# Kernel tuning notes

Hardware: AMD Instinct MI355X
Metric: run time of the kernel (lower is better)

## Reference

```python
import jax, jax.numpy as jnp
import numpy as np

B, N, L, D, H, NLAYERS, V = 8, 1024, 16, 256, 4, 2, 32000
DH = D // H  # per-head dim


def setup_inputs() -> dict:
    key = jax.random.key(0)
    ks = jax.random.split(key, 7)
    cfg_adj = jax.random.randint(ks[0], (B, N, N), 0, 2, dtype=jnp.int32)
    cfg_nodes = jax.random.randint(ks[1], (B, N, L), 0, V, dtype=jnp.int32)
    cfg_len = jax.random.randint(ks[2], (B,), 1, N + 1, dtype=jnp.int32)
    emb = jax.random.normal(ks[3], (V, D), jnp.float32) * 0.02
    # xavier-ish scale for per-head projections and attention vectors
    W = jax.random.normal(ks[4], (NLAYERS, H, D, DH), jnp.float32) * np.float32(np.sqrt(2.0 / (D + DH)))
    a_src = jax.random.normal(ks[5], (NLAYERS, H, DH), jnp.float32) * 0.1
    a_dst = jax.random.normal(ks[6], (NLAYERS, H, DH), jnp.float32) * 0.1
    ln_scale = jnp.ones((NLAYERS, D), jnp.float32)
    ln_bias = jnp.zeros((NLAYERS, D), jnp.float32)
    return {"cfg_adj": cfg_adj, "cfg_nodes": cfg_nodes, "cfg_len": cfg_len,
            "emb": emb, "W": W, "a_src": a_src, "a_dst": a_dst,
            "ln_scale": ln_scale, "ln_bias": ln_bias}


def _layer_norm(x, scale, bias, eps=1e-5):
    mu = jnp.mean(x, axis=-1, keepdims=True)
    var = jnp.var(x, axis=-1, keepdims=True)
    return (x - mu) * jax.lax.rsqrt(var + eps) * scale + bias


def reference(cfg_adj, cfg_nodes, cfg_len, emb, W, a_src, a_dst, ln_scale, ln_bias):
    # node features: mean over token embeddings (dropout is identity in eval)
    node_feat = emb[cfg_nodes].mean(axis=2)                       # (B,N,D)
    # add self-loops once (repeated add+clamp in the original is idempotent)
    adj = jnp.minimum(cfg_adj + jnp.eye(N, dtype=cfg_adj.dtype)[None], 1)
    neg_mask = (adj == 0)[:, None]                                # (B,1,N,N)
    h = node_feat
    for l in range(NLAYERS):
        Wh = jnp.einsum('bnd,hdk->bhnk', h, W[l])                 # (B,H,N,DH)
        src = jnp.einsum('bhnk,hk->bhn', Wh, a_src[l])            # (B,H,N)
        dst = jnp.einsum('bhnk,hk->bhn', Wh, a_dst[l])            # (B,H,N)
        e = jax.nn.leaky_relu(src[:, :, :, None] + dst[:, :, None, :], 0.2)
        e = jnp.where(neg_mask, jnp.float32(-1e9), e)             # masked fill
        alpha = jax.nn.softmax(e, axis=-1)                        # (B,H,N,N)
        h_prime = jnp.einsum('bhnm,bhmk->bhnk', alpha, Wh)        # (B,H,N,DH)
        h_cat = jnp.transpose(h_prime, (0, 2, 1, 3)).reshape(B, N, D)
        h = _layer_norm(h + h_cat, ln_scale[l], ln_bias[l])
    return h, cfg_len
```

## Files before the change

kernel.cpp:

```cpp
#include <hip/hip_runtime.h>
#include <math.h>

#define B 8
#define N 1024
#define L 16
#define D 256
#define H 4
#define DH 64
#define NLAYERS 2
#define V 32000

typedef __attribute__((ext_vector_type(8))) short short8;
typedef __attribute__((ext_vector_type(4))) float f32x4;

union U8 { uint4 u; short8 s; };

__device__ inline unsigned short f2bf(float x) {
    unsigned u = __float_as_uint(x);
    u = (u + 0x7fff + ((u >> 16) & 1)) >> 16;
    return (unsigned short)u;
}
__device__ inline float bf2f(unsigned short x) {
    return __uint_as_float(((unsigned)x) << 16);
}


#define PACK_BLK 2048
#define WT_BLK   (NLAYERS * H * 4)
#define EMB_BLK  500
#define PRE1_GRID (PACK_BLK + WT_BLK + EMB_BLK + 1)

__global__ __launch_bounds__(256) void k_pre1(const int* __restrict__ adj,
                                              const float* __restrict__ W,
                                              const int* __restrict__ len,
                                              const float* __restrict__ emb,
                                              unsigned long long* __restrict__ pack,
                                              unsigned short* __restrict__ WT_sw,
                                              unsigned short* __restrict__ emb_bf,
                                              float* __restrict__ out_len) {
    int bid = blockIdx.x;
    int t = threadIdx.x;
    if (bid < PACK_BLK) {
        int row = bid * 4 + (t >> 6);
        int lane = t & 63;
        int n = row & (N - 1);
        const int* arow = adj + (long)row * N;
        unsigned long long* prow = pack + (size_t)row * 16;
        int g16 = lane & 15;
#pragma unroll
        for (int it = 0; it < 4; ++it) {
            int m0 = it * 256 + lane * 4;
            int4 a = *(const int4*)(arow + m0);
            unsigned nib = (unsigned)((a.x != 0) || (m0 == n))
                         | ((unsigned)((a.y != 0) || (m0 + 1 == n)) << 1)
                         | ((unsigned)((a.z != 0) || (m0 + 2 == n)) << 2)
                         | ((unsigned)((a.w != 0) || (m0 + 3 == n)) << 3);
            unsigned long long v = (unsigned long long)nib << (g16 * 4);
            v |= __shfl_xor(v, 1, 64);
            v |= __shfl_xor(v, 2, 64);
            v |= __shfl_xor(v, 4, 64);
            v |= __shfl_xor(v, 8, 64);
            if (g16 == 0) prow[it * 4 + (lane >> 4)] = v;
        }
    } else if (bid < PACK_BLK + WT_BLK) {
        int idx = bid - PACK_BLK;
        int lh = idx >> 2, q = idx & 3;
        const float* Wl = W + (size_t)lh * D * DH;
        int dh = t & 63;
        int d0 = q * 64 + (t >> 6) * 16;
#pragma unroll
        for (int i = 0; i < 16; ++i) {
            int d = d0 + i;
            WT_sw[(((size_t)lh * 8 + (d >> 5)) * 64 + dh) * 32 + (d & 31)] = f2bf(Wl[(size_t)d * DH + dh]);
        }
    } else if (bid < PACK_BLK + WT_BLK + EMB_BLK) {
        size_t base = (size_t)(bid - PACK_BLK - WT_BLK) * 16384 + (size_t)t * 4;
#pragma unroll
        for (int i = 0; i < 16; ++i) {
            float4 v = *(const float4*)&emb[base + (size_t)i * 1024];
            ushort4 o;
            o.x = f2bf(v.x); o.y = f2bf(v.y); o.z = f2bf(v.z); o.w = f2bf(v.w);
            *(ushort4*)&emb_bf[base + (size_t)i * 1024] = o;
        }
    } else {
        if (t < B) out_len[t] = (float)len[t];
    }
}

__global__ __launch_bounds__(256) void k_nodefeat(const int* __restrict__ nodes,
                                                  const unsigned short* __restrict__ emb_bf,
                                                  float* __restrict__ h,
                                                  unsigned short* __restrict__ h_sw) {
    int row = blockIdx.x * 8 + (threadIdx.x >> 5);
    int lane32 = threadIdx.x & 31;
    int d8 = lane32 * 8;
    const int* np = nodes + row * L;
    float s[8] = {};
#pragma unroll
    for (int l = 0; l < L; ++l) {
        short8 v = *(const short8*)&emb_bf[(size_t)np[l] * D + d8];
#pragma unroll
        for (int k = 0; k < 8; ++k) s[k] += bf2f((unsigned short)v[k]);
    }
#pragma unroll
    for (int k = 0; k < 8; ++k) s[k] *= (1.0f / L);
    *(float4*)&h[(size_t)row * D + d8] = make_float4(s[0], s[1], s[2], s[3]);
    *(float4*)&h[(size_t)row * D + d8 + 4] = make_float4(s[4], s[5], s[6], s[7]);
    int b = row >> 10, n = row & 1023;
    unsigned short o[8];
#pragma unroll
    for (int k = 0; k < 8; ++k) o[k] = f2bf(s[k]);
    *(short8*)&h_sw[(((size_t)b * 64 + (n >> 4)) * 8 + (d8 >> 5)) * 512 + (n & 15) * 32 + (d8 & 31)] =
        *(short8*)o;
}

__global__ __launch_bounds__(256) void k_wh(const unsigned short* __restrict__ h_sw,
                                            const unsigned short* __restrict__ WT_l,
                                            const float* __restrict__ asrc_l,
                                            const float* __restrict__ adst_l,
                                            unsigned short* __restrict__ WhT,
                                            float* __restrict__ srcv,
                                            float* __restrict__ dstv) {
    __shared__ float red[4][16][68];
    int bt = blockIdx.x;
    int hh = blockIdx.y;
    int b = bt >> 6;
    int nt = bt & 63;
    int n0 = nt * 16;
    int tid = threadIdx.x;
    int w = tid >> 6, lane = tid & 63;
    int rowLane = lane & 15, quad = lane >> 4;
    int bh = b * H + hh;
    const unsigned short* abase = h_sw + (((size_t)b * 64 + nt) * 8) * 512 + rowLane * 32 + quad * 8;
    const unsigned short* bbase = WT_l + ((size_t)hh * 8) * 2048 + rowLane * 32 + quad * 8;
    f32x4 acc[4] = {};
#pragma unroll
    for (int kk = 0; kk < 2; ++kk) {
        int kc = w * 2 + kk;
        short8 af = *(const short8*)(abase + kc * 512);
#pragma unroll
        for (int c = 0; c < 4; ++c) {
            short8 bf = *(const short8*)(bbase + kc * 2048 + c * 512);
            acc[c] = __builtin_amdgcn_mfma_f32_16x16x32_bf16(af, bf, acc[c], 0, 0, 0);
        }
    }
#pragma unroll
    for (int c = 0; c < 4; ++c)
#pragma unroll
        for (int r = 0; r < 4; ++r)
            red[w][quad * 4 + r][c * 16 + rowLane] = acc[c][r];
    __syncthreads();
    int dh = tid >> 2, j4 = tid & 3;
    float v[4];
#pragma unroll
    for (int i = 0; i < 4; ++i)
        v[i] = red[0][j4 * 4 + i][dh] + red[1][j4 * 4 + i][dh] + red[2][j4 * 4 + i][dh] + red[3][j4 * 4 + i][dh];
    ushort4 o;
    o.x = f2bf(v[0]); o.y = f2bf(v[1]); o.z = f2bf(v[2]); o.w = f2bf(v[3]);
    *(ushort4*)&WhT[(((size_t)bh * 32 + (n0 >> 5)) * 64 + dh) * 32 + (n0 & 31) + j4 * 4] = o;
    float as = asrc_l[hh * DH + dh];
    float ad = adst_l[hh * DH + dh];
    float* ps = &red[0][0][0];
    float* pd = ps + 16 * 68;
    __syncthreads();
#pragma unroll
    for (int i = 0; i < 4; ++i) {
        ps[(j4 * 4 + i) * 68 + dh] = v[i] * as;
        pd[(j4 * 4 + i) * 68 + dh] = v[i] * ad;
    }
    __syncthreads();
    int nl = tid >> 4, g = tid & 15;
    float4 s4 = *(float4*)&ps[nl * 68 + g * 4];
    float4 t4 = *(float4*)&pd[nl * 68 + g * 4];
    float s1 = s4.x + s4.y + s4.z + s4.w;
    float d1 = t4.x + t4.y + t4.z + t4.w;
#pragma unroll
    for (int off = 8; off; off >>= 1) {
        s1 += __shfl_xor(s1, off, 16);
        d1 += __shfl_xor(d1, off, 16);
    }
    if (g == 0) {
        srcv[bh * N + n0 + nl] = s1;
        dstv[bh * N + n0 + nl] = d1;
    }
}

__global__ __launch_bounds__(256) void k_attn(const unsigned long long* __restrict__ pack,
                                              const float* __restrict__ srcv,
                                              const float* __restrict__ dstv,
                                              const unsigned short* __restrict__ WhT,
                                              float* __restrict__ hp) {
    __shared__ float red[4][16][68];
    __shared__ float ssum[4][16];
    float* dsts = &red[0][0][0];

    int tid = threadIdx.x;
    int bt = blockIdx.x;
    int bh = bt >> 6;
    int n0 = (bt & 63) * 16;
    int b = bh >> 2;
    int w = tid >> 6, lane = tid & 63;
    int rowLane = lane & 15, quad = lane >> 4;
    int n = n0 + rowLane;

    {
        float4 v = *(const float4*)(dstv + bh * N + w * 256 + lane * 4);
        *(float4*)(dsts + w * 256 + lane * 4) = v;
    }
    const uint4* pbp = (const uint4*)((const unsigned char*)(pack + ((size_t)(b * N + n)) * 16) + w * 32);
    uint4 pbv0 = pbp[0];
    uint4 pbv1 = pbp[1];
    float src = srcv[bh * N + n];
    float mx = src > 0.f ? src : 0.2f * src;

    unsigned words[8] = {pbv0.x, pbv0.y, pbv0.z, pbv0.w, pbv1.x, pbv1.y, pbv1.z, pbv1.w};
    const unsigned short* wbase = WhT + ((size_t)bh * 32) * 2048 + rowLane * 32 + quad * 8;
    f32x4 acc[4] = {};
    float sum0 = 0.f, sum1 = 0.f;
#pragma unroll
    for (int t2 = 0; t2 < 8; ++t2) {
        unsigned bits = (words[t2] >> (quad * 8)) & 0xffu;
        float4 d0 = *(const float4*)(dsts + w * 256 + t2 * 32 + quad * 8);
        float4 d1 = *(const float4*)(dsts + w * 256 + t2 * 32 + quad * 8 + 4);
        float dd[8] = {d0.x, d0.y, d0.z, d0.w, d1.x, d1.y, d1.z, d1.w};
        unsigned pk[4];
#pragma unroll
        for (int j2 = 0; j2 < 4; ++j2) {
            float ea = src + dd[2 * j2];
            float eb = src + dd[2 * j2 + 1];
            ea = ea > 0.f ? ea : 0.2f * ea;
            eb = eb > 0.f ? eb : 0.2f * eb;
            float pa = ((bits >> (2 * j2)) & 1) ? __expf(ea - mx) : 0.f;
            float pb = ((bits >> (2 * j2 + 1)) & 1) ? __expf(eb - mx) : 0.f;
            sum0 += pa; sum1 += pb;
            pk[j2] = (__float_as_uint(pb) & 0xffff0000u) | (__float_as_uint(pa) >> 16);
        }
        U8 u; u.u = make_uint4(pk[0], pk[1], pk[2], pk[3]);
        short8 af = u.s;
        const unsigned short* tb = wbase + (size_t)(w * 8 + t2) * 2048;
        acc[0] = __builtin_amdgcn_mfma_f32_16x16x32_bf16(af, *(const short8*)(tb + 0 * 512), acc[0], 0, 0, 0);
        acc[1] = __builtin_amdgcn_mfma_f32_16x16x32_bf16(af, *(const short8*)(tb + 1 * 512), acc[1], 0, 0, 0);
        acc[2] = __builtin_amdgcn_mfma_f32_16x16x32_bf16(af, *(const short8*)(tb + 2 * 512), acc[2], 0, 0, 0);
        acc[3] = __builtin_amdgcn_mfma_f32_16x16x32_bf16(af, *(const short8*)(tb + 3 * 512), acc[3], 0, 0, 0);
    }
    float sum = sum0 + sum1;
    sum += __shfl_xor(sum, 16, 64);
    sum += __shfl_xor(sum, 32, 64);
    if (quad == 0) ssum[w][rowLane] = sum;
    __syncthreads();
#pragma unroll
    for (int c = 0; c < 4; ++c)
#pragma unroll
        for (int r = 0; r < 4; ++r)
            red[w][quad * 4 + r][c * 16 + rowLane] = acc[c][r];
    __syncthreads();
    int row = tid >> 4, col4 = (tid & 15) * 4;
    float4 s = make_float4(0.f, 0.f, 0.f, 0.f);
#pragma unroll
    for (int ww = 0; ww < 4; ++ww) {
        float4 v = *(const float4*)&red[ww][row][col4];
        s.x += v.x; s.y += v.y; s.z += v.z; s.w += v.w;
    }
    float invr = 1.0f / (ssum[0][row] + ssum[1][row] + ssum[2][row] + ssum[3][row]);
    s.x *= invr; s.y *= invr; s.z *= invr; s.w *= invr;
    *(float4*)&hp[((size_t)bh * N + n0 + row) * DH + col4] = s;
}

__global__ __launch_bounds__(256) void k_ln(const float* __restrict__ h,
                                            const float* __restrict__ hp,
                                            const float* __restrict__ scale,
                                            const float* __restrict__ bias,
                                            float* __restrict__ out,
                                            unsigned short* __restrict__ h_sw,
                                            int layer, int has_next) {
    __shared__ float red[8];
    int bn = blockIdx.x;
    int b = bn >> 10, n = bn & 1023;
    int c = threadIdx.x;
    int hh = c >> 6, k = c & 63;
    float x = h[(size_t)bn * D + c] + hp[((size_t)(b * H + hh) * N + n) * DH + k];
    float s = x, s2 = x * x;
#pragma unroll
    for (int off = 32; off; off >>= 1) {
        s += __shfl_xor(s, off, 64);
        s2 += __shfl_xor(s2, off, 64);
    }
    int w = c >> 6, lane = c & 63;
    if (lane == 0) { red[w] = s; red[4 + w] = s2; }
    __syncthreads();
    s = red[0] + red[1] + red[2] + red[3];
    s2 = red[4] + red[5] + red[6] + red[7];
    float mu = s * (1.0f / D);
    float var = s2 * (1.0f / D) - mu * mu;
    float r = rsqrtf(var + 1e-5f);
    float y = (x - mu) * r * scale[layer * D + c] + bias[layer * D + c];
    out[(size_t)bn * D + c] = y;
    if (has_next)
        h_sw[(((size_t)b * 64 + (n >> 4)) * 8 + (c >> 5)) * 512 + (n & 15) * 32 + (c & 31)] = f2bf(y);
}

extern "C" void kernel_launch(void* const* d_in, const int* in_sizes, int n_in,
                              void* d_out, int out_size, void* d_ws, size_t ws_size,
                              hipStream_t stream) {
    const int* cfg_adj = (const int*)d_in[0];
    const int* cfg_nodes = (const int*)d_in[1];
    const int* cfg_len = (const int*)d_in[2];
    const float* emb = (const float*)d_in[3];
    const float* W = (const float*)d_in[4];
    const float* a_src = (const float*)d_in[5];
    const float* a_dst = (const float*)d_in[6];
    const float* ln_scale = (const float*)d_in[7];
    const float* ln_bias = (const float*)d_in[8];
    float* out = (float*)d_out;
    float* ws = (float*)d_ws;

    float* h = ws;
    float* hp = h + (size_t)B * N * D;
    float* srcv = hp + (size_t)B * H * N * DH;
    float* dstv = srcv + (size_t)B * H * N;
    unsigned short* h_sw = (unsigned short*)(dstv + (size_t)B * H * N);
    unsigned short* WhT = h_sw + (size_t)B * N * D;
    unsigned short* WT_sw = WhT + (size_t)B * H * DH * N;
    unsigned short* emb_bf = WT_sw + (size_t)NLAYERS * H * DH * D;
    unsigned long long* pack = (unsigned long long*)(emb_bf + (size_t)V * D);

    k_pre1<<<PRE1_GRID, 256, 0, stream>>>(cfg_adj, W, cfg_len, emb, pack, WT_sw,
                                          emb_bf, out + (size_t)B * N * D);
    k_nodefeat<<<B * N / 8, 256, 0, stream>>>(cfg_nodes, emb_bf, h, h_sw);
    for (int l = 0; l < NLAYERS; ++l) {
        k_wh<<<dim3(B * 64, H), 256, 0, stream>>>(
            h_sw, WT_sw + (size_t)l * H * 8 * 2048,
            a_src + (size_t)l * H * DH, a_dst + (size_t)l * H * DH,
            WhT, srcv, dstv);
        k_attn<<<B * H * 64, 256, 0, stream>>>(pack, srcv, dstv, WhT, hp);
        k_ln<<<B * N, 256, 0, stream>>>(h, hp, ln_scale, ln_bias,
                                        (l == NLAYERS - 1) ? out : h, h_sw,
                                        l, l < NLAYERS - 1 ? 1 : 0);
    }
}
```

Before: 203.1 us.

## Fuse node-feature gather with Wh projection and attention with layernorm

```diff
diff --git a/kernel.cpp b/kernel.cpp
--- a/kernel.cpp
+++ b/kernel.cpp
@@ -87,141 +87,177 @@
     }
 }
 
-__global__ __launch_bounds__(256) void k_nodefeat(const int* __restrict__ nodes,
-                                                  const unsigned short* __restrict__ emb_bf,
-                                                  float* __restrict__ h,
-                                                  unsigned short* __restrict__ h_sw) {
-    int row = blockIdx.x * 8 + (threadIdx.x >> 5);
-    int lane32 = threadIdx.x & 31;
-    int d8 = lane32 * 8;
-    const int* np = nodes + row * L;
-    float s[8] = {};
-#pragma unroll
-    for (int l = 0; l < L; ++l) {
-        short8 v = *(const short8*)&emb_bf[(size_t)np[l] * D + d8];
-#pragma unroll
-        for (int k = 0; k < 8; ++k) s[k] += bf2f((unsigned short)v[k]);
-    }
-#pragma unroll
-    for (int k = 0; k < 8; ++k) s[k] *= (1.0f / L);
-    *(float4*)&h[(size_t)row * D + d8] = make_float4(s[0], s[1], s[2], s[3]);
-    *(float4*)&h[(size_t)row * D + d8 + 4] = make_float4(s[4], s[5], s[6], s[7]);
-    int b = row >> 10, n = row & 1023;
-    unsigned short o[8];
-#pragma unroll
-    for (int k = 0; k < 8; ++k) o[k] = f2bf(s[k]);
-    *(short8*)&h_sw[(((size_t)b * 64 + (n >> 4)) * 8 + (d8 >> 5)) * 512 + (n & 15) * 32 + (d8 & 31)] =
-        *(short8*)o;
-}
-
-__global__ __launch_bounds__(256) void k_wh(const unsigned short* __restrict__ h_sw,
-                                            const unsigned short* __restrict__ WT_l,
-                                            const float* __restrict__ asrc_l,
-                                            const float* __restrict__ adst_l,
-                                            unsigned short* __restrict__ WhT,
-                                            float* __restrict__ srcv,
-                                            float* __restrict__ dstv) {
-    __shared__ float red[4][16][68];
-    int bt = blockIdx.x;
-    int hh = blockIdx.y;
-    int b = bt >> 6;
-    int nt = bt & 63;
-    int n0 = nt * 16;
-    int tid = threadIdx.x;
-    int w = tid >> 6, lane = tid & 63;
+__device__ inline void wh_epilogue(float (*wtmp)[16][68], const f32x4* acc,
+                                   const float* asrc_l, const float* adst_l,
+                                   unsigned short* WhT, float* srcv, float* dstv,
+                                   int b, int n0, int tid) {
+    int hh = tid >> 6, lane = tid & 63;
     int rowLane = lane & 15, quad = lane >> 4;
     int bh = b * H + hh;
+    float as[4], ad[4];
+#pragma unroll
+    for (int c = 0; c < 4; ++c) {
+        as[c] = asrc_l[hh * DH + c * 16 + rowLane];
+        ad[c] = adst_l[hh * DH + c * 16 + rowLane];
+    }
+#pragma unroll
+    for (int rr = 0; rr < 4; ++rr) {
+        float sp = acc[0][rr] * as[0] + acc[1][rr] * as[1] + acc[2][rr] * as[2] + acc[3][rr] * as[3];
+        float dp = acc[0][rr] * ad[0] + acc[1][rr] * ad[1] + acc[2][rr] * ad[2] + acc[3][rr] * ad[3];
+#pragma unroll
+        for (int off = 8; off; off >>= 1) {
+            sp += __shfl_xor(sp, off, 16);
+            dp += __shfl_xor(dp, off, 16);
+        }
+        if (rowLane == 0) {
+            srcv[(size_t)bh * N + n0 + quad * 4 + rr] = sp;
+            dstv[(size_t)bh * N + n0 + quad * 4 + rr] = dp;
+        }
+    }
+#pragma unroll
+    for (int c = 0; c < 4; ++c)
+#pragma unroll
+        for (int rr = 0; rr < 4; ++rr)
+            wtmp[hh][quad * 4 + rr][c * 16 + rowLane] = acc[c][rr];
+    __syncthreads();
+    int hh2 = tid >> 6, dh = tid & 63;
+    int bh2 = b * H + hh2;
+#pragma unroll
+    for (int j4 = 0; j4 < 4; ++j4) {
+        ushort4 o;
+        o.x = f2bf(wtmp[hh2][j4 * 4 + 0][dh]);
+        o.y = f2bf(wtmp[hh2][j4 * 4 + 1][dh]);
+        o.z = f2bf(wtmp[hh2][j4 * 4 + 2][dh]);
+        o.w = f2bf(wtmp[hh2][j4 * 4 + 3][dh]);
+        *(ushort4*)&WhT[(((size_t)bh2 * 32 + (n0 >> 5)) * 64 + dh) * 32 + (n0 & 31) + j4 * 4] = o;
+    }
+}
+
+__global__ __launch_bounds__(256) void k_feat_wh(const int* __restrict__ nodes,
+                                                 const unsigned short* __restrict__ emb_bf,
+                                                 const unsigned short* __restrict__ WT_l,
+                                                 const float* __restrict__ asrc_l,
+                                                 const float* __restrict__ adst_l,
+                                                 float* __restrict__ h,
+                                                 unsigned short* __restrict__ WhT,
+                                                 float* __restrict__ srcv,
+                                                 float* __restrict__ dstv) {
+    __shared__ int ndl[256];
+    __shared__ unsigned short a_lds[8][16][40];
+    __shared__ float wtmp[4][16][68];
+    int bt = blockIdx.x;
+    int b = bt >> 6, nt = bt & 63, n0 = nt * 16;
+    int tid = threadIdx.x;
+    ndl[tid] = nodes[((size_t)(b * N + n0)) * L + tid];
+    __syncthreads();
+    int r = tid >> 4, g = tid & 15;
+    float s[16] = {};
+#pragma unroll
+    for (int l = 0; l < L; ++l) {
+        int tok = ndl[r * 16 + l];
+        short8 v0 = *(const short8*)&emb_bf[(size_t)tok * D + g * 16];
+        short8 v1 = *(const short8*)&emb_bf[(size_t)tok * D + g * 16 + 8];
+#pragma unroll
+        for (int k = 0; k < 8; ++k) {
+            s[k] += bf2f((unsigned short)v0[k]);
+            s[8 + k] += bf2f((unsigned short)v1[k]);
+        }
+    }
+#pragma unroll
+    for (int k = 0; k < 16; ++k) s[k] *= (1.0f / L);
+    float* hrow = h + ((size_t)(b * N + n0 + r)) * D + g * 16;
+    *(float4*)(hrow + 0) = make_float4(s[0], s[1], s[2], s[3]);
+    *(float4*)(hrow + 4) = make_float4(s[4], s[5], s[6], s[7]);
+    *(float4*)(hrow + 8) = make_float4(s[8], s[9], s[10], s[11]);
+    *(float4*)(hrow + 12) = make_float4(s[12], s[13], s[14], s[15]);
+    unsigned short ob[16];
+#pragma unroll
+    for (int k = 0; k < 16; ++k) ob[k] = f2bf(s[k]);
+    *(short8*)&a_lds[g >> 1][r][(g & 1) * 16] = *(short8*)&ob[0];
+    *(short8*)&a_lds[g >> 1][r][(g & 1) * 16 + 8] = *(short8*)&ob[8];
+    __syncthreads();
+    int hh = tid >> 6, lane = tid & 63;
+    int rowLane = lane & 15, quad = lane >> 4;
+    const unsigned short* bbase = WT_l + ((size_t)hh * 8) * 2048 + rowLane * 32 + quad * 8;
+    f32x4 acc[4] = {};
+#pragma unroll
+    for (int kc = 0; kc < 8; ++kc) {
+        short8 af = *(const short8*)&a_lds[kc][rowLane][quad * 8];
+#pragma unroll
+        for (int c = 0; c < 4; ++c)
+            acc[c] = __builtin_amdgcn_mfma_f32_16x16x32_bf16(af, *(const short8*)(bbase + kc * 2048 + c * 512), acc[c], 0, 0, 0);
+    }
+    wh_epilogue(wtmp, acc, asrc_l, adst_l, WhT, srcv, dstv, b, n0, tid);
+}
+
+__global__ __launch_bounds__(256) void k_wh1(const unsigned short* __restrict__ h_sw,
+                                             const unsigned short* __restrict__ WT_l,
+                                             const float* __restrict__ asrc_l,
+                                             const float* __restrict__ adst_l,
+                                             unsigned short* __restrict__ WhT,
+                                             float* __restrict__ srcv,
+                                             float* __restrict__ dstv) {
+    __shared__ float wtmp[4][16][68];
+    int bt = blockIdx.x;
+    int b = bt >> 6, nt = bt & 63, n0 = nt * 16;
+    int tid = threadIdx.x;
+    int hh = tid >> 6, lane = tid & 63;
+    int rowLane = lane & 15, quad = lane >> 4;
     const unsigned short* abase = h_sw + (((size_t)b * 64 + nt) * 8) * 512 + rowLane * 32 + quad * 8;
     const unsigned short* bbase = WT_l + ((size_t)hh * 8) * 2048 + rowLane * 32 + quad * 8;
     f32x4 acc[4] = {};
 #pragma unroll
-    for (int kk = 0; kk < 2; ++kk) {
-        int kc = w * 2 + kk;
+    for (int kc = 0; kc < 8; ++kc) {
         short8 af = *(const short8*)(abase + kc * 512);
 #pragma unroll
-        for (int c = 0; c < 4; ++c) {
-            short8 bf = *(const short8*)(bbase + kc * 2048 + c * 512);
-            acc[c] = __builtin_amdgcn_mfma_f32_16x16x32_bf16(af, bf, acc[c], 0, 0, 0);
-        }
-    }
-#pragma unroll
-    for (int c = 0; c < 4; ++c)
-#pragma unroll
-        for (int r = 0; r < 4; ++r)
-            red[w][quad * 4 + r][c * 16 + rowLane] = acc[c][r];
-    __syncthreads();
-    int dh = tid >> 2, j4 = tid & 3;
-    float v[4];
-#pragma unroll
-    for (int i = 0; i < 4; ++i)
-        v[i] = red[0][j4 * 4 + i][dh] + red[1][j4 * 4 + i][dh] + red[2][j4 * 4 + i][dh] + red[3][j4 * 4 + i][dh];
-    ushort4 o;
-    o.x = f2bf(v[0]); o.y = f2bf(v[1]); o.z = f2bf(v[2]); o.w = f2bf(v[3]);
-    *(ushort4*)&WhT[(((size_t)bh * 32 + (n0 >> 5)) * 64 + dh) * 32 + (n0 & 31) + j4 * 4] = o;
-    float as = asrc_l[hh * DH + dh];
-    float ad = adst_l[hh * DH + dh];
-    float* ps = &red[0][0][0];
-    float* pd = ps + 16 * 68;
-    __syncthreads();
+        for (int c = 0; c < 4; ++c)
+            acc[c] = __builtin_amdgcn_mfma_f32_16x16x32_bf16(af, *(const short8*)(bbase + kc * 2048 + c * 512), acc[c], 0, 0, 0);
+    }
+    wh_epilogue(wtmp, acc, asrc_l, adst_l, WhT, srcv, dstv, b, n0, tid);
+}
+
+__global__ __launch_bounds__(256) void k_attn_ln(const unsigned long long* __restrict__ pack,
+                                                 const float* __restrict__ srcv,
+                                                 const float* __restrict__ dstv,
+                                                 const unsigned short* __restrict__ WhT,
+                                                 const float* __restrict__ h_in,
+                                                 const float* __restrict__ scale_l,
+                                                 const float* __restrict__ bias_l,
+                                                 float* __restrict__ out_f32,
+                                                 unsigned short* __restrict__ h_sw_out,
+                                                 int has_next) {
+    __shared__ float dsts[4][1024];
+    __shared__ float xbuf[16][272];
+    int bt = blockIdx.x;
+    int b = bt >> 6, nt = bt & 63, n0 = nt * 16;
+    int tid = threadIdx.x;
+    int hh = tid >> 6, lane = tid & 63;
+    int rowLane = lane & 15, quad = lane >> 4;
+    int bh = b * H + hh;
+    int n = n0 + rowLane;
+
 #pragma unroll
     for (int i = 0; i < 4; ++i) {
-        ps[(j4 * 4 + i) * 68 + dh] = v[i] * as;
-        pd[(j4 * 4 + i) * 68 + dh] = v[i] * ad;
-    }
-    __syncthreads();
-    int nl = tid >> 4, g = tid & 15;
-    float4 s4 = *(float4*)&ps[nl * 68 + g * 4];
-    float4 t4 = *(float4*)&pd[nl * 68 + g * 4];
-    float s1 = s4.x + s4.y + s4.z + s4.w;
-    float d1 = t4.x + t4.y + t4.z + t4.w;
-#pragma unroll
-    for (int off = 8; off; off >>= 1) {
-        s1 += __shfl_xor(s1, off, 16);
-        d1 += __shfl_xor(d1, off, 16);
-    }
-    if (g == 0) {
-        srcv[bh * N + n0 + nl] = s1;
-        dstv[bh * N + n0 + nl] = d1;
-    }
-}
-
-__global__ __launch_bounds__(256) void k_attn(const unsigned long long* __restrict__ pack,
-                                              const float* __restrict__ srcv,
-                                              const float* __restrict__ dstv,
-                                              const unsigned short* __restrict__ WhT,
-                                              float* __restrict__ hp) {
-    __shared__ float red[4][16][68];
-    __shared__ float ssum[4][16];
-    float* dsts = &red[0][0][0];
-
-    int tid = threadIdx.x;
-    int bt = blockIdx.x;
-    int bh = bt >> 6;
-    int n0 = (bt & 63) * 16;
-    int b = bh >> 2;
-    int w = tid >> 6, lane = tid & 63;
-    int rowLane = lane & 15, quad = lane >> 4;
-    int n = n0 + rowLane;
-
-    {
-        float4 v = *(const float4*)(dstv + bh * N + w * 256 + lane * 4);
-        *(float4*)(dsts + w * 256 + lane * 4) = v;
-    }
-    const uint4* pbp = (const uint4*)((const unsigned char*)(pack + ((size_t)(b * N + n)) * 16) + w * 32);
-    uint4 pbv0 = pbp[0];
-    uint4 pbv1 = pbp[1];
-    float src = srcv[bh * N + n];
+        float4 v = *(const float4*)(dstv + (size_t)bh * N + i * 256 + lane * 4);
+        *(float4*)&dsts[hh][i * 256 + lane * 4] = v;
+    }
+    const uint4* pbp = (const uint4*)(pack + ((size_t)(b * N + n)) * 16);
+    uint4 pw[8];
+#pragma unroll
+    for (int i = 0; i < 8; ++i) pw[i] = pbp[i];
+    float src = srcv[(size_t)bh * N + n];
     float mx = src > 0.f ? src : 0.2f * src;
 
-    unsigned words[8] = {pbv0.x, pbv0.y, pbv0.z, pbv0.w, pbv1.x, pbv1.y, pbv1.z, pbv1.w};
-    const unsigned short* wbase = WhT + ((size_t)bh * 32) * 2048 + rowLane * 32 + quad * 8;
+    const unsigned short* wbase = WhT + (size_t)bh * 65536 + rowLane * 32 + quad * 8;
     f32x4 acc[4] = {};
     float sum0 = 0.f, sum1 = 0.f;
 #pragma unroll
-    for (int t2 = 0; t2 < 8; ++t2) {
-        unsigned bits = (words[t2] >> (quad * 8)) & 0xffu;
-        float4 d0 = *(const float4*)(dsts + w * 256 + t2 * 32 + quad * 8);
-        float4 d1 = *(const float4*)(dsts + w * 256 + t2 * 32 + quad * 8 + 4);
+    for (int t2 = 0; t2 < 32; ++t2) {
+        uint4 q = pw[t2 >> 2];
+        unsigned w32 = (t2 & 3) == 0 ? q.x : (t2 & 3) == 1 ? q.y : (t2 & 3) == 2 ? q.z : q.w;
+        unsigned bits = (w32 >> (quad * 8)) & 0xffu;
+        float4 d0 = *(const float4*)&dsts[hh][t2 * 32 + quad * 8];
+        float4 d1 = *(const float4*)&dsts[hh][t2 * 32 + quad * 8 + 4];
         float dd[8] = {d0.x, d0.y, d0.z, d0.w, d1.x, d1.y, d1.z, d1.w};
         unsigned pk[4];
 #pragma unroll
@@ -237,7 +273,7 @@
         }
         U8 u; u.u = make_uint4(pk[0], pk[1], pk[2], pk[3]);
         short8 af = u.s;
-        const unsigned short* tb = wbase + (size_t)(w * 8 + t2) * 2048;
+        const unsigned short* tb = wbase + (size_t)t2 * 2048;
         acc[0] = __builtin_amdgcn_mfma_f32_16x16x32_bf16(af, *(const short8*)(tb + 0 * 512), acc[0], 0, 0, 0);
         acc[1] = __builtin_amdgcn_mfma_f32_16x16x32_bf16(af, *(const short8*)(tb + 1 * 512), acc[1], 0, 0, 0);
         acc[2] = __builtin_amdgcn_mfma_f32_16x16x32_bf16(af, *(const short8*)(tb + 2 * 512), acc[2], 0, 0, 0);
@@ -246,57 +282,57 @@
     float sum = sum0 + sum1;
     sum += __shfl_xor(sum, 16, 64);
     sum += __shfl_xor(sum, 32, 64);
-    if (quad == 0) ssum[w][rowLane] = sum;
+#pragma unroll
+    for (int rr = 0; rr < 4; ++rr) {
+        float Sr = __shfl(sum, quad * 4 + rr, 16);
+        float inv = 1.0f / Sr;
+#pragma unroll
+        for (int c = 0; c < 4; ++c)
+            xbuf[quad * 4 + rr][hh * 64 + c * 16 + rowLane] = acc[c][rr] * inv;
+    }
     __syncthreads();
-#pragma unroll
-    for (int c = 0; c < 4; ++c)
-#pragma unroll
-        for (int r = 0; r < 4; ++r)
-            red[w][quad * 4 + r][c * 16 + rowLane] = acc[c][r];
-    __syncthreads();
-    int row = tid >> 4, col4 = (tid & 15) * 4;
-    float4 s = make_float4(0.f, 0.f, 0.f, 0.f);
-#pragma unroll
-    for (int ww = 0; ww < 4; ++ww) {
-        float4 v = *(const float4*)&red[ww][row][col4];
-        s.x += v.x; s.y += v.y; s.z += v.z; s.w += v.w;
-    }
-    float invr = 1.0f / (ssum[0][row] + ssum[1][row] + ssum[2][row] + ssum[3][row]);
-    s.x *= invr; s.y *= invr; s.z *= invr; s.w *= invr;
-    *(float4*)&hp[((size_t)bh * N + n0 + row) * DH + col4] = s;
-}
-
-__global__ __launch_bounds__(256) void k_ln(const float* __restrict__ h,
-                                            const float* __restrict__ hp,
-                                            const float* __restrict__ scale,
-                                            const float* __restrict__ bias,
-                                            float* __restrict__ out,
-                                            unsigned short* __restrict__ h_sw,
-                                            int layer, int has_next) {
-    __shared__ float red[8];
-    int bn = blockIdx.x;
-    int b = bn >> 10, n = bn & 1023;
-    int c = threadIdx.x;
-    int hh = c >> 6, k = c & 63;
-    float x = h[(size_t)bn * D + c] + hp[((size_t)(b * H + hh) * N + n) * DH + k];
-    float s = x, s2 = x * x;
-#pragma unroll
-    for (int off = 32; off; off >>= 1) {
-        s += __shfl_xor(s, off, 64);
-        s2 += __shfl_xor(s2, off, 64);
-    }
-    int w = c >> 6, lane = c & 63;
-    if (lane == 0) { red[w] = s; red[4 + w] = s2; }
-    __syncthreads();
-    s = red[0] + red[1] + red[2] + red[3];
-    s2 = red[4] + red[5] + red[6] + red[7];
-    float mu = s * (1.0f / D);
+    int r = tid >> 4, g = tid & 15;
+    size_t bn = (size_t)b * N + n0 + r;
+    float x[16];
+    const float* hr = h_in + bn * D + g * 16;
+#pragma unroll
+    for (int i4 = 0; i4 < 4; ++i4) {
+        float4 xv = *(const float4*)&xbuf[r][g * 16 + i4 * 4];
+        float4 hv = *(const float4*)(hr + i4 * 4);
+        x[i4 * 4 + 0] = xv.x + hv.x;
+        x[i4 * 4 + 1] = xv.y + hv.y;
+        x[i4 * 4 + 2] = xv.z + hv.z;
+        x[i4 * 4 + 3] = xv.w + hv.w;
+    }
+    float s1 = 0.f, s2 = 0.f;
+#pragma unroll
+    for (int i = 0; i < 16; ++i) { s1 += x[i]; s2 += x[i] * x[i]; }
+#pragma unroll
+    for (int off = 8; off; off >>= 1) {
+        s1 += __shfl_xor(s1, off, 16);
+        s2 += __shfl_xor(s2, off, 16);
+    }
+    float mu = s1 * (1.0f / D);
     float var = s2 * (1.0f / D) - mu * mu;
-    float r = rsqrtf(var + 1e-5f);
-    float y = (x - mu) * r * scale[layer * D + c] + bias[layer * D + c];
-    out[(size_t)bn * D + c] = y;
-    if (has_next)
-        h_sw[(((size_t)b * 64 + (n >> 4)) * 8 + (c >> 5)) * 512 + (n & 15) * 32 + (c & 31)] = f2bf(y);
+    float rstd = rsqrtf(var + 1e-5f);
+    const float* sc = scale_l + g * 16;
+    const float* bi = bias_l + g * 16;
+    float y[16];
+#pragma unroll
+    for (int i = 0; i < 16; ++i) y[i] = (x[i] - mu) * rstd * sc[i] + bi[i];
+    float* orow = out_f32 + bn * D + g * 16;
+    *(float4*)(orow + 0) = make_float4(y[0], y[1], y[2], y[3]);
+    *(float4*)(orow + 4) = make_float4(y[4], y[5], y[6], y[7]);
+    *(float4*)(orow + 8) = make_float4(y[8], y[9], y[10], y[11]);
+    *(float4*)(orow + 12) = make_float4(y[12], y[13], y[14], y[15]);
+    if (has_next) {
+        unsigned short ob[16];
+#pragma unroll
+        for (int i = 0; i < 16; ++i) ob[i] = f2bf(y[i]);
+        unsigned short* hswp = h_sw_out + (((size_t)b * 64 + nt) * 8 + (g >> 1)) * 512 + r * 32 + (g & 1) * 16;
+        *(short8*)(hswp + 0) = *(short8*)&ob[0];
+        *(short8*)(hswp + 8) = *(short8*)&ob[8];
+    }
 }
 
 extern "C" void kernel_launch(void* const* d_in, const int* in_sizes, int n_in,
@@ -315,8 +351,7 @@
     float* ws = (float*)d_ws;
 
     float* h = ws;
-    float* hp = h + (size_t)B * N * D;
-    float* srcv = hp + (size_t)B * H * N * DH;
+    float* srcv = h + (size_t)B * N * D;
     float* dstv = srcv + (size_t)B * H * N;
     unsigned short* h_sw = (unsigned short*)(dstv + (size_t)B * H * N);
     unsigned short* WhT = h_sw + (size_t)B * N * D;
@@ -326,15 +361,13 @@
 
     k_pre1<<<PRE1_GRID, 256, 0, stream>>>(cfg_adj, W, cfg_len, emb, pack, WT_sw,
                                           emb_bf, out + (size_t)B * N * D);
-    k_nodefeat<<<B * N / 8, 256, 0, stream>>>(cfg_nodes, emb_bf, h, h_sw);
-    for (int l = 0; l < NLAYERS; ++l) {
-        k_wh<<<dim3(B * 64, H), 256, 0, stream>>>(
-            h_sw, WT_sw + (size_t)l * H * 8 * 2048,
-            a_src + (size_t)l * H * DH, a_dst + (size_t)l * H * DH,
-            WhT, srcv, dstv);
-        k_attn<<<B * H * 64, 256, 0, stream>>>(pack, srcv, dstv, WhT, hp);
-        k_ln<<<B * N, 256, 0, stream>>>(h, hp, ln_scale, ln_bias,
-                                        (l == NLAYERS - 1) ? out : h, h_sw,
-                                        l, l < NLAYERS - 1 ? 1 : 0);
-    }
-}
+    k_feat_wh<<<B * 64, 256, 0, stream>>>(cfg_nodes, emb_bf, WT_sw,
+                                          a_src, a_dst, h, WhT, srcv, dstv);
+    k_attn_ln<<<B * 64, 256, 0, stream>>>(pack, srcv, dstv, WhT, h,
+                                          ln_scale, ln_bias, h, h_sw, 1);
+    k_wh1<<<B * 64, 256, 0, stream>>>(h_sw, WT_sw + (size_t)H * 8 * 2048,
+                                      a_src + (size_t)H * DH, a_dst + (size_t)H * DH,
+                                      WhT, srcv, dstv);
+    k_attn_ln<<<B * 64, 256, 0, stream>>>(pack, srcv, dstv, WhT, h,
+                                          ln_scale + D, ln_bias + D, out, (unsigned short*)0, 0);
+}
```

After: 258.2 us. 27.1% more time.

## Fuse node-feature gather into preprocessing and carry residual/attention outputs in bf16

Applied to the files above, without the earlier changes.

```diff
diff --git a/kernel.cpp b/kernel.cpp
--- a/kernel.cpp
+++ b/kernel.cpp
@@ -27,16 +27,17 @@
 
 #define PACK_BLK 2048
 #define WT_BLK   (NLAYERS * H * 4)
-#define EMB_BLK  500
-#define PRE1_GRID (PACK_BLK + WT_BLK + EMB_BLK + 1)
+#define FEAT_BLK 2048
+#define PRE1_GRID (PACK_BLK + WT_BLK + FEAT_BLK + 1)
 
 __global__ __launch_bounds__(256) void k_pre1(const int* __restrict__ adj,
                                               const float* __restrict__ W,
                                               const int* __restrict__ len,
                                               const float* __restrict__ emb,
+                                              const int* __restrict__ nodes,
                                               unsigned long long* __restrict__ pack,
                                               unsigned short* __restrict__ WT_sw,
-                                              unsigned short* __restrict__ emb_bf,
+                                              unsigned short* __restrict__ h_sw,
                                               float* __restrict__ out_len) {
     int bid = blockIdx.x;
     int t = threadIdx.x;
@@ -73,45 +74,25 @@
             int d = d0 + i;
             WT_sw[(((size_t)lh * 8 + (d >> 5)) * 64 + dh) * 32 + (d & 31)] = f2bf(Wl[(size_t)d * DH + dh]);
         }
-    } else if (bid < PACK_BLK + WT_BLK + EMB_BLK) {
-        size_t base = (size_t)(bid - PACK_BLK - WT_BLK) * 16384 + (size_t)t * 4;
-#pragma unroll
-        for (int i = 0; i < 16; ++i) {
-            float4 v = *(const float4*)&emb[base + (size_t)i * 1024];
-            ushort4 o;
-            o.x = f2bf(v.x); o.y = f2bf(v.y); o.z = f2bf(v.z); o.w = f2bf(v.w);
-            *(ushort4*)&emb_bf[base + (size_t)i * 1024] = o;
-        }
+    } else if (bid < PACK_BLK + WT_BLK + FEAT_BLK) {
+        int row = (bid - PACK_BLK - WT_BLK) * 4 + (t >> 6);
+        int lane = t & 63;
+        int d4 = lane * 4;
+        const int* np = nodes + row * L;
+        float4 s = make_float4(0.f, 0.f, 0.f, 0.f);
+#pragma unroll
+        for (int l = 0; l < L; ++l) {
+            float4 v = *(const float4*)&emb[(size_t)np[l] * D + d4];
+            s.x += v.x; s.y += v.y; s.z += v.z; s.w += v.w;
+        }
+        s.x *= (1.0f / L); s.y *= (1.0f / L); s.z *= (1.0f / L); s.w *= (1.0f / L);
+        int b = row >> 10, n = row & 1023;
+        ushort4 o;
+        o.x = f2bf(s.x); o.y = f2bf(s.y); o.z = f2bf(s.z); o.w = f2bf(s.w);
+        *(ushort4*)&h_sw[(((size_t)b * 64 + (n >> 4)) * 8 + (d4 >> 5)) * 512 + (n & 15) * 32 + (d4 & 31)] = o;
     } else {
         if (t < B) out_len[t] = (float)len[t];
     }
-}
-
-__global__ __launch_bounds__(256) void k_nodefeat(const int* __restrict__ nodes,
-                                                  const unsigned short* __restrict__ emb_bf,
-                                                  float* __restrict__ h,
-                                                  unsigned short* __restrict__ h_sw) {
-    int row = blockIdx.x * 8 + (threadIdx.x >> 5);
-    int lane32 = threadIdx.x & 31;
-    int d8 = lane32 * 8;
-    const int* np = nodes + row * L;
-    float s[8] = {};
-#pragma unroll
-    for (int l = 0; l < L; ++l) {
-        short8 v = *(const short8*)&emb_bf[(size_t)np[l] * D + d8];
-#pragma unroll
-        for (int k = 0; k < 8; ++k) s[k] += bf2f((unsigned short)v[k]);
-    }
-#pragma unroll
-    for (int k = 0; k < 8; ++k) s[k] *= (1.0f / L);
-    *(float4*)&h[(size_t)row * D + d8] = make_float4(s[0], s[1], s[2], s[3]);
-    *(float4*)&h[(size_t)row * D + d8 + 4] = make_float4(s[4], s[5], s[6], s[7]);
-    int b = row >> 10, n = row & 1023;
-    unsigned short o[8];
-#pragma unroll
-    for (int k = 0; k < 8; ++k) o[k] = f2bf(s[k]);
-    *(short8*)&h_sw[(((size_t)b * 64 + (n >> 4)) * 8 + (d8 >> 5)) * 512 + (n & 15) * 32 + (d8 & 31)] =
-        *(short8*)o;
 }
 
 __global__ __launch_bounds__(256) void k_wh(const unsigned short* __restrict__ h_sw,
@@ -189,7 +170,7 @@
                                               const float* __restrict__ srcv,
                                               const float* __restrict__ dstv,
                                               const unsigned short* __restrict__ WhT,
-                                              float* __restrict__ hp) {
+                                              unsigned short* __restrict__ hp_bf) {
     __shared__ float red[4][16][68];
     __shared__ float ssum[4][16];
     float* dsts = &red[0][0][0];
@@ -262,23 +243,26 @@
         s.x += v.x; s.y += v.y; s.z += v.z; s.w += v.w;
     }
     float invr = 1.0f / (ssum[0][row] + ssum[1][row] + ssum[2][row] + ssum[3][row]);
-    s.x *= invr; s.y *= invr; s.z *= invr; s.w *= invr;
-    *(float4*)&hp[((size_t)bh * N + n0 + row) * DH + col4] = s;
-}
-
-__global__ __launch_bounds__(256) void k_ln(const float* __restrict__ h,
-                                            const float* __restrict__ hp,
+    ushort4 o;
+    o.x = f2bf(s.x * invr); o.y = f2bf(s.y * invr);
+    o.z = f2bf(s.z * invr); o.w = f2bf(s.w * invr);
+    *(ushort4*)&hp_bf[((size_t)bh * N + n0 + row) * DH + col4] = o;
+}
+
+__global__ __launch_bounds__(256) void k_ln(const unsigned short* __restrict__ h_sw_in,
+                                            const unsigned short* __restrict__ hp_bf,
                                             const float* __restrict__ scale,
                                             const float* __restrict__ bias,
                                             float* __restrict__ out,
-                                            unsigned short* __restrict__ h_sw,
-                                            int layer, int has_next) {
+                                            unsigned short* __restrict__ h_sw_out,
+                                            int layer, int is_final) {
     __shared__ float red[8];
     int bn = blockIdx.x;
     int b = bn >> 10, n = bn & 1023;
     int c = threadIdx.x;
     int hh = c >> 6, k = c & 63;
-    float x = h[(size_t)bn * D + c] + hp[((size_t)(b * H + hh) * N + n) * DH + k];
+    size_t swidx = (((size_t)b * 64 + (n >> 4)) * 8 + (c >> 5)) * 512 + (n & 15) * 32 + (c & 31);
+    float x = bf2f(h_sw_in[swidx]) + bf2f(hp_bf[((size_t)(b * H + hh) * N + n) * DH + k]);
     float s = x, s2 = x * x;
 #pragma unroll
     for (int off = 32; off; off >>= 1) {
@@ -294,9 +278,8 @@
     float var = s2 * (1.0f / D) - mu * mu;
     float r = rsqrtf(var + 1e-5f);
     float y = (x - mu) * r * scale[layer * D + c] + bias[layer * D + c];
-    out[(size_t)bn * D + c] = y;
-    if (has_next)
-        h_sw[(((size_t)b * 64 + (n >> 4)) * 8 + (c >> 5)) * 512 + (n & 15) * 32 + (c & 31)] = f2bf(y);
+    if (is_final) out[(size_t)bn * D + c] = y;
+    else h_sw_out[swidx] = f2bf(y);
 }
 
 extern "C" void kernel_launch(void* const* d_in, const int* in_sizes, int n_in,
@@ -314,27 +297,23 @@
     float* out = (float*)d_out;
     float* ws = (float*)d_ws;
 
-    float* h = ws;
-    float* hp = h + (size_t)B * N * D;
-    float* srcv = hp + (size_t)B * H * N * DH;
+    float* srcv = ws;
     float* dstv = srcv + (size_t)B * H * N;
     unsigned short* h_sw = (unsigned short*)(dstv + (size_t)B * H * N);
     unsigned short* WhT = h_sw + (size_t)B * N * D;
     unsigned short* WT_sw = WhT + (size_t)B * H * DH * N;
-    unsigned short* emb_bf = WT_sw + (size_t)NLAYERS * H * DH * D;
-    unsigned long long* pack = (unsigned long long*)(emb_bf + (size_t)V * D);
-
-    k_pre1<<<PRE1_GRID, 256, 0, stream>>>(cfg_adj, W, cfg_len, emb, pack, WT_sw,
-                                          emb_bf, out + (size_t)B * N * D);
-    k_nodefeat<<<B * N / 8, 256, 0, stream>>>(cfg_nodes, emb_bf, h, h_sw);
+    unsigned short* hp_bf = WT_sw + (size_t)NLAYERS * H * DH * D;
+    unsigned long long* pack = (unsigned long long*)(hp_bf + (size_t)B * H * N * DH);
+
+    k_pre1<<<PRE1_GRID, 256, 0, stream>>>(cfg_adj, W, cfg_len, emb, cfg_nodes,
+                                          pack, WT_sw, h_sw, out + (size_t)B * N * D);
     for (int l = 0; l < NLAYERS; ++l) {
         k_wh<<<dim3(B * 64, H), 256, 0, stream>>>(
             h_sw, WT_sw + (size_t)l * H * 8 * 2048,
             a_src + (size_t)l * H * DH, a_dst + (size_t)l * H * DH,
             WhT, srcv, dstv);
-        k_attn<<<B * H * 64, 256, 0, stream>>>(pack, srcv, dstv, WhT, hp);
-        k_ln<<<B * N, 256, 0, stream>>>(h, hp, ln_scale, ln_bias,
-                                        (l == NLAYERS - 1) ? out : h, h_sw,
-                                        l, l < NLAYERS - 1 ? 1 : 0);
-    }
-}
+        k_attn<<<B * H * 64, 256, 0, stream>>>(pack, srcv, dstv, WhT, hp_bf);
+        k_ln<<<B * N, 256, 0, stream>>>(h_sw, hp_bf, ln_scale, ln_bias,
+                                        out, h_sw, l, l == NLAYERS - 1 ? 1 : 0);
+    }
+}
```

New measurement: 196.3 us. 1.03x faster.
